# Kernel tuning notes

Hardware: AMD Instinct MI355X
Metric: run time of the kernel (lower is better)

## Reference

```python
import jax, jax.numpy as jnp
import numpy as np

B, N, D = 8, 2048, 256      # batch, tokens, model dim (= out_token_dims)
S = 128                     # query_key_dims
H = int(2.0 * D)            # expansion_factor * D = 512
EPS = 1e-5


def setup_inputs() -> dict:
    key = jax.random.key(0)
    ks = jax.random.split(key, 4)
    x = jax.random.normal(ks[0], (B, N, D), dtype=jnp.float32)
    g = jnp.ones((), jnp.float32)                                # ScaleNorm gain
    W_uv = jax.random.normal(ks[1], (D, 2 * H + S), jnp.float32) * 0.02
    b_uv = jnp.zeros((2 * H + S,), jnp.float32)
    gamma = jnp.ones((2, S), jnp.float32)                        # OffsetScale scale
    beta = jnp.zeros((2, S), jnp.float32)                        # OffsetScale offset
    W_o = jax.random.normal(ks[2], (H, D), jnp.float32) * 0.02
    b_o = jnp.zeros((D,), jnp.float32)
    return {"x": x, "g": g, "W_uv": W_uv, "b_uv": b_uv,
            "gamma": gamma, "beta": beta, "W_o": W_o, "b_o": b_o}


def reference(x, g, W_uv, b_uv, gamma, beta, W_o, b_o):
    d = x.shape[-1]
    # ScaleNorm: x / max(||x|| / sqrt(d), eps) * g
    norm = jnp.linalg.norm(x, axis=-1, keepdims=True) * jax.lax.rsqrt(jnp.float32(d))
    xn = x / jnp.maximum(norm, EPS) * g
    # fused uv projection + SiLU
    uv = jax.nn.silu(jnp.einsum('bnd,de->bne', xn, W_uv) + b_uv)
    u = uv[..., :H]            # gate branch        [B,N,H]
    v = uv[..., H:2 * H]       # value branch       [B,N,H]
    base = uv[..., 2 * H:]     # shared q/k base    [B,N,S]
    # OffsetScale heads=2 -> q, k (cheap per-dim affine)
    q = base * gamma[0] + beta[0]
    k = base * gamma[1] + beta[1]
    # single-head scores + ReLU^2 attention activation
    qk = jnp.einsum('bns,bms->bnm', q, k) * jax.lax.rsqrt(jnp.float32(S))
    attn = jnp.square(jax.nn.relu(qk))
    # gate * (attn @ v), then output projection back to D
    gated = u * jnp.einsum('bnm,bmh->bnh', attn, v)
    return jnp.einsum('bnh,hd->bnd', gated, W_o) + b_o
```

## Files before the change

### kernel.cpp

```cpp
#include <hip/hip_runtime.h>
#include <math.h>

#define BB 8
#define NN 2048
#define DD 256
#define SS 128
#define HH 512
#define EE 1152

typedef short bf16x8 __attribute__((ext_vector_type(8)));
typedef float f32x4 __attribute__((ext_vector_type(4)));

__device__ __forceinline__ short f2bf(float f) {
    union { float f; unsigned u; } a; a.f = f;
    unsigned r = a.u + 0x7FFFu + ((a.u >> 16) & 1u);
    return (short)(r >> 16);
}
__device__ __forceinline__ float bf2f(short s) {
    union { unsigned u; float f; } a; a.u = ((unsigned)(unsigned short)s) << 16;
    return a.f;
}

__global__ __launch_bounds__(256) void k_pre(
        const float* __restrict__ x, const float* __restrict__ gp,
        short* __restrict__ xn,
        const float* __restrict__ Wuv, const float* __restrict__ Wo,
        short* __restrict__ Wuv_t, short* __restrict__ Wo_t) {
    int bid = blockIdx.x;
    if (bid < 4096) {
        int wave = threadIdx.x >> 6, lane = threadIdx.x & 63;
        long row = (long)bid * 4 + wave;
        float4 xv = ((const float4*)(x + row * DD))[lane];
        float ss = xv.x*xv.x + xv.y*xv.y + xv.z*xv.z + xv.w*xv.w;
        #pragma unroll
        for (int off = 32; off > 0; off >>= 1) ss += __shfl_down(ss, off);
        ss = __shfl(ss, 0);
        float norm = sqrtf(ss) * 0.0625f;
        float scale = gp[0] / fmaxf(norm, 1e-5f);
        short4 o;
        o.x = f2bf(xv.x * scale); o.y = f2bf(xv.y * scale);
        o.z = f2bf(xv.z * scale); o.w = f2bf(xv.w * scale);
        ((short4*)(xn + row * DD))[lane] = o;
    } else {
        int idx = (bid - 4096) * 256 + threadIdx.x;
        if (idx < DD * EE) {
            int d = idx / EE, e = idx % EE;
            Wuv_t[e * DD + d] = f2bf(Wuv[idx]);
        }
        int i2 = idx - DD * EE;
        if (i2 >= 0 && i2 < HH * DD) {
            int h = i2 / DD, d = i2 % DD;
            Wo_t[d * HH + h] = f2bf(Wo[i2]);
        }
    }
}

__global__ __launch_bounds__(256) void k_gemm1(
        const short* __restrict__ xn, const short* __restrict__ Wuv_t,
        const float* __restrict__ b_uv,
        const float* __restrict__ gamma, const float* __restrict__ beta,
        short* __restrict__ u, short* __restrict__ v,
        short* __restrict__ q, short* __restrict__ k) {
    __shared__ short As[64][72];
    __shared__ short Bs[64][72];
    int m0 = blockIdx.x * 64, n0 = blockIdx.y * 64;
    int t = threadIdx.x, w = t >> 6, lane = t & 63;
    int wr = w & 1, wc = w >> 1, l16 = lane & 15, quad = lane >> 4;
    int srow = t >> 3, sch = (t & 7) * 8;
    f32x4 acc[2][2] = {};
    for (int k0 = 0; k0 < DD; k0 += 64) {
        __syncthreads();
        *(bf16x8*)&As[srow][sch]    = *(const bf16x8*)&xn[(long)(m0+srow)*DD + k0 + sch];
        *(bf16x8*)&As[srow+32][sch] = *(const bf16x8*)&xn[(long)(m0+srow+32)*DD + k0 + sch];
        *(bf16x8*)&Bs[srow][sch]    = *(const bf16x8*)&Wuv_t[(long)(n0+srow)*DD + k0 + sch];
        *(bf16x8*)&Bs[srow+32][sch] = *(const bf16x8*)&Wuv_t[(long)(n0+srow+32)*DD + k0 + sch];
        __syncthreads();
        #pragma unroll
        for (int kk = 0; kk < 2; kk++) {
            bf16x8 a0 = *(const bf16x8*)&As[wr*32 +      l16][kk*32 + quad*8];
            bf16x8 a1 = *(const bf16x8*)&As[wr*32 + 16 + l16][kk*32 + quad*8];
            bf16x8 b0 = *(const bf16x8*)&Bs[wc*32 +      l16][kk*32 + quad*8];
            bf16x8 b1 = *(const bf16x8*)&Bs[wc*32 + 16 + l16][kk*32 + quad*8];
            acc[0][0] = __builtin_amdgcn_mfma_f32_16x16x32_bf16(a0, b0, acc[0][0], 0,0,0);
            acc[0][1] = __builtin_amdgcn_mfma_f32_16x16x32_bf16(a0, b1, acc[0][1], 0,0,0);
            acc[1][0] = __builtin_amdgcn_mfma_f32_16x16x32_bf16(a1, b0, acc[1][0], 0,0,0);
            acc[1][1] = __builtin_amdgcn_mfma_f32_16x16x32_bf16(a1, b1, acc[1][1], 0,0,0);
        }
    }
    #pragma unroll
    for (int mt = 0; mt < 2; mt++)
    #pragma unroll
    for (int nt = 0; nt < 2; nt++)
    #pragma unroll
    for (int r = 0; r < 4; r++) {
        int gm = m0 + wr*32 + mt*16 + quad*4 + r;
        int ge = n0 + wc*32 + nt*16 + l16;
        float val = acc[mt][nt][r] + b_uv[ge];
        val = val / (1.0f + __expf(-val));
        if (ge < HH) {
            u[(long)gm*HH + ge] = f2bf(val);
        } else if (ge < 2*HH) {
            v[(long)gm*HH + (ge - HH)] = f2bf(val);
        } else {
            int si = ge - 2*HH;
            q[(long)gm*SS + si] = f2bf(val * gamma[si]      + beta[si]);
            k[(long)gm*SS + si] = f2bf(val * gamma[SS + si] + beta[SS + si]);
        }
    }
}

__global__ __launch_bounds__(256) void k_vfrag(
        const short* __restrict__ v, short* __restrict__ vfrag) {
    __shared__ short tile[32][520];
    int mt = blockIdx.x, b = blockIdx.y;
    int t = threadIdx.x;
    const short* vb = v + ((long)b * NN + mt * 32) * HH;
    #pragma unroll
    for (int i = 0; i < 8; i++) {
        int c = t + i * 256, r = c >> 6, co = (c & 63) * 8;
        *(bf16x8*)&tile[r][co] = *(const bf16x8*)&vb[(long)r * HH + co];
    }
    __syncthreads();
    short* dstb = vfrag + (((long)b * 64 + mt) * 32) * 512;
    #pragma unroll
    for (int i = 0; i < 8; i++) {
        int c = t + i * 256, ht = c >> 6, l = c & 63;
        int quad = l >> 4, l16 = l & 15;
        bf16x8 o;
        #pragma unroll
        for (int e = 0; e < 8; e++) o[e] = tile[quad*8 + e][ht*16 + l16];
        *(bf16x8*)&dstb[(long)ht * 512 + l * 8] = o;
    }
}

__global__ __launch_bounds__(512, 2) void k_attn(
        const short* __restrict__ q, const short* __restrict__ k,
        const short* __restrict__ vfrag, const short* __restrict__ u,
        short* __restrict__ gated) {
    __shared__ short ks[2][32][136];
    __shared__ short Ps[2][64][40];
    int b = blockIdx.x & 7;
    int i0 = (blockIdx.x >> 3) * 64;
    int t = threadIdx.x, w = t >> 6, lane = t & 63;
    int l16 = lane & 15, quad = lane >> 4;
    int qt = w >> 1, mt = w & 1;
    const short* qb  = q + ((long)b * NN + i0) * SS;
    const short* kb  = k + (long)b * NN * SS;
    const short* vfb = vfrag + (long)b * 64 * 32 * 512;
    const float RS = 0.08838834764831845f;

    int krow = t >> 4, kch = (t & 15) * 8;

    bf16x8 qf[4];
    #pragma unroll
    for (int kc = 0; kc < 4; kc++)
        qf[kc] = *(const bf16x8*)&qb[(long)(qt*16 + l16)*SS + kc*32 + quad*8];

    *(bf16x8*)&ks[0][krow][kch] = *(const bf16x8*)&kb[(long)krow*SS + kch];
    bf16x8 kpre = *(const bf16x8*)&kb[(long)(32 + krow)*SS + kch];
    __syncthreads();

    f32x4 acc[16] = {};
    for (int it = 0; it < NN/32; it++) {
        int p = it & 1;
        int m0 = it * 32;
        int mnext = (m0 + 64 < NN) ? m0 + 64 : m0;
        bf16x8 knext = *(const bf16x8*)&kb[(long)(mnext + krow)*SS + kch];
        bf16x8 vf[4];
        #pragma unroll
        for (int jj = 0; jj < 4; jj++)
            vf[jj] = *(const bf16x8*)&vfb[((long)it*32 + (w*4 + jj))*512 + lane*8];
        f32x4 sc = {};
        #pragma unroll
        for (int kc = 0; kc < 4; kc++) {
            bf16x8 kf = *(const bf16x8*)&ks[p][mt*16 + l16][kc*32 + quad*8];
            sc = __builtin_amdgcn_mfma_f32_16x16x32_bf16(kf, qf[kc], sc, 0,0,0);
        }
        short4 pw;
        {
            float s0 = fmaxf(sc[0]*RS, 0.f), s1 = fmaxf(sc[1]*RS, 0.f);
            float s2 = fmaxf(sc[2]*RS, 0.f), s3 = fmaxf(sc[3]*RS, 0.f);
            pw.x = f2bf(s0*s0); pw.y = f2bf(s1*s1);
            pw.z = f2bf(s2*s2); pw.w = f2bf(s3*s3);
        }
        *(short4*)&Ps[p][qt*16 + l16][mt*16 + quad*4] = pw;
        *(bf16x8*)&ks[p^1][krow][kch] = kpre;
        kpre = knext;
        __syncthreads();
        bf16x8 af[4];
        #pragma unroll
        for (int qq2 = 0; qq2 < 4; qq2++)
            af[qq2] = *(const bf16x8*)&Ps[p][qq2*16 + l16][quad*8];
        #pragma unroll
        for (int jj = 0; jj < 4; jj++)
            #pragma unroll
            for (int qq2 = 0; qq2 < 4; qq2++)
                acc[qq2*4 + jj] = __builtin_amdgcn_mfma_f32_16x16x32_bf16(
                    af[qq2], vf[jj], acc[qq2*4 + jj], 0,0,0);
    }

    long rowbase = (long)b * NN + i0;
    #pragma unroll
    for (int qq2 = 0; qq2 < 4; qq2++)
    #pragma unroll
    for (int jj = 0; jj < 4; jj++) {
        int gh = (w*4 + jj)*16 + l16;
        #pragma unroll
        for (int r = 0; r < 4; r++) {
            long grow = rowbase + qq2*16 + quad*4 + r;
            float uval = bf2f(u[grow * HH + gh]);
            gated[grow * HH + gh] = f2bf(acc[qq2*4 + jj][r] * uval);
        }
    }
}

__global__ __launch_bounds__(256) void k_gemm2(
        const short* __restrict__ gated, const short* __restrict__ Wo_t,
        const float* __restrict__ b_o, float* __restrict__ out) {
    __shared__ short As[64][72];
    __shared__ short Bs[64][72];
    int m0 = blockIdx.x * 64, n0 = blockIdx.y * 64;
    int t = threadIdx.x, w = t >> 6, lane = t & 63;
    int wr = w & 1, wc = w >> 1, l16 = lane & 15, quad = lane >> 4;
    int srow = t >> 3, sch = (t & 7) * 8;
    f32x4 acc[2][2] = {};
    for (int k0 = 0; k0 < HH; k0 += 64) {
        __syncthreads();
        *(bf16x8*)&As[srow][sch]    = *(const bf16x8*)&gated[(long)(m0+srow)*HH + k0 + sch];
        *(bf16x8*)&As[srow+32][sch] = *(const bf16x8*)&gated[(long)(m0+srow+32)*HH + k0 + sch];
        *(bf16x8*)&Bs[srow][sch]    = *(const bf16x8*)&Wo_t[(long)(n0+srow)*HH + k0 + sch];
        *(bf16x8*)&Bs[srow+32][sch] = *(const bf16x8*)&Wo_t[(long)(n0+srow+32)*HH + k0 + sch];
        __syncthreads();
        #pragma unroll
        for (int kk = 0; kk < 2; kk++) {
            bf16x8 a0 = *(const bf16x8*)&As[wr*32 +      l16][kk*32 + quad*8];
            bf16x8 a1 = *(const bf16x8*)&As[wr*32 + 16 + l16][kk*32 + quad*8];
            bf16x8 b0 = *(const bf16x8*)&Bs[wc*32 +      l16][kk*32 + quad*8];
            bf16x8 b1 = *(const bf16x8*)&Bs[wc*32 + 16 + l16][kk*32 + quad*8];
            acc[0][0] = __builtin_amdgcn_mfma_f32_16x16x32_bf16(a0, b0, acc[0][0], 0,0,0);
            acc[0][1] = __builtin_amdgcn_mfma_f32_16x16x32_bf16(a0, b1, acc[0][1], 0,0,0);
            acc[1][0] = __builtin_amdgcn_mfma_f32_16x16x32_bf16(a1, b0, acc[1][0], 0,0,0);
            acc[1][1] = __builtin_amdgcn_mfma_f32_16x16x32_bf16(a1, b1, acc[1][1], 0,0,0);
        }
    }
    #pragma unroll
    for (int mt = 0; mt < 2; mt++)
    #pragma unroll
    for (int nt = 0; nt < 2; nt++)
    #pragma unroll
    for (int r = 0; r < 4; r++) {
        int gm = m0 + wr*32 + mt*16 + quad*4 + r;
        int gd = n0 + wc*32 + nt*16 + l16;
        out[(long)gm*DD + gd] = acc[mt][nt][r] + b_o[gd];
    }
}

extern "C" void kernel_launch(void* const* d_in, const int* in_sizes, int n_in,
                              void* d_out, int out_size, void* d_ws, size_t ws_size,
                              hipStream_t stream) {
    const float* x     = (const float*)d_in[0];
    const float* g     = (const float*)d_in[1];
    const float* Wuv   = (const float*)d_in[2];
    const float* b_uv  = (const float*)d_in[3];
    const float* gamma = (const float*)d_in[4];
    const float* beta  = (const float*)d_in[5];
    const float* Wo    = (const float*)d_in[6];
    const float* b_o   = (const float*)d_in[7];
    float* out = (float*)d_out;

    short* ws    = (short*)d_ws;
    short* xn    = ws;
    short* Wuv_t = xn    + (long)16384 * 256;
    short* Wo_t  = Wuv_t + (long)1152 * 256;
    short* u     = Wo_t  + (long)256 * 512;
    short* v     = u     + (long)16384 * 512;
    short* vfrag = v     + (long)16384 * 512;
    short* qq    = vfrag + (long)16384 * 512;
    short* kk    = qq    + (long)16384 * 128;
    short* gated = kk    + (long)16384 * 128;

    k_pre<<<5760, 256, 0, stream>>>(x, g, xn, Wuv, Wo, Wuv_t, Wo_t);
    k_gemm1<<<dim3(256, 18), 256, 0, stream>>>(xn, Wuv_t, b_uv, gamma, beta, u, v, qq, kk);
    k_vfrag<<<dim3(64, 8), 256, 0, stream>>>(v, vfrag);
    k_attn<<<256, 512, 0, stream>>>(qq, kk, vfrag, u, gated);
    k_gemm2<<<dim3(256, 4), 256, 0, stream>>>(gated, Wo_t, b_o, out);
}
```

Measured before the change: 174.1 us.

## Tile weight transposes, enlarge GEMM tiles with direct-to-LDS loads, double-step attention loop

The weight-transpose path now goes through a 32x32 shared-memory tile, so both reads and writes are coalesced. Both projection GEMMs move from 64x64 to 128x128 tiles, load operands with global_load_lds straight into unpadded LDS, and issue 16 MFMAs per wave per k-step. The attention loop handles two 32-key chunks per iteration and prefetches V fragments one step ahead, which halves the number of barriers. The unpadded LDS layout may cause bank conflicts, and the larger tiles launch fewer blocks (1152 for gemm1, 256 for gemm2), which can lower occupancy.

Measured after the change: 182.3 us. +4.7%, slower.

```diff
diff --git a/kernel.cpp b/kernel.cpp
--- a/kernel.cpp
+++ b/kernel.cpp
@@ -20,15 +20,22 @@
     union { unsigned u; float f; } a; a.u = ((unsigned)(unsigned short)s) << 16;
     return a.f;
 }
+__device__ __forceinline__ void gl_lds16(const short* g, short* l) {
+    __builtin_amdgcn_global_load_lds(
+        (const __attribute__((address_space(1))) void*)g,
+        (__attribute__((address_space(3))) void*)l, 16, 0, 0);
+}
 
 __global__ __launch_bounds__(256) void k_pre(
         const float* __restrict__ x, const float* __restrict__ gp,
         short* __restrict__ xn,
         const float* __restrict__ Wuv, const float* __restrict__ Wo,
         short* __restrict__ Wuv_t, short* __restrict__ Wo_t) {
+    __shared__ float tile[32][33];
     int bid = blockIdx.x;
+    int t = threadIdx.x;
     if (bid < 4096) {
-        int wave = threadIdx.x >> 6, lane = threadIdx.x & 63;
+        int wave = t >> 6, lane = t & 63;
         long row = (long)bid * 4 + wave;
         float4 xv = ((const float4*)(x + row * DD))[lane];
         float ss = xv.x*xv.x + xv.y*xv.y + xv.z*xv.z + xv.w*xv.w;
@@ -41,16 +48,33 @@
         o.x = f2bf(xv.x * scale); o.y = f2bf(xv.y * scale);
         o.z = f2bf(xv.z * scale); o.w = f2bf(xv.w * scale);
         ((short4*)(xn + row * DD))[lane] = o;
+    } else if (bid < 4384) {
+        int bid2 = bid - 4096;
+        int et = bid2 % 36, dt = bid2 / 36;
+        #pragma unroll
+        for (int i = 0; i < 4; i++) {
+            int idx = t + i*256, r = idx >> 5, c = idx & 31;
+            tile[r][c] = Wuv[(long)(dt*32 + r)*EE + et*32 + c];
+        }
+        __syncthreads();
+        #pragma unroll
+        for (int i = 0; i < 4; i++) {
+            int idx = t + i*256, r = idx >> 5, c = idx & 31;
+            Wuv_t[(long)(et*32 + r)*DD + dt*32 + c] = f2bf(tile[c][r]);
+        }
     } else {
-        int idx = (bid - 4096) * 256 + threadIdx.x;
-        if (idx < DD * EE) {
-            int d = idx / EE, e = idx % EE;
-            Wuv_t[e * DD + d] = f2bf(Wuv[idx]);
-        }
-        int i2 = idx - DD * EE;
-        if (i2 >= 0 && i2 < HH * DD) {
-            int h = i2 / DD, d = i2 % DD;
-            Wo_t[d * HH + h] = f2bf(Wo[i2]);
+        int bid3 = bid - 4384;
+        int ht = bid3 % 16, dt = bid3 / 16;
+        #pragma unroll
+        for (int i = 0; i < 4; i++) {
+            int idx = t + i*256, r = idx >> 5, c = idx & 31;
+            tile[r][c] = Wo[(long)(ht*32 + r)*DD + dt*32 + c];
+        }
+        __syncthreads();
+        #pragma unroll
+        for (int i = 0; i < 4; i++) {
+            int idx = t + i*256, r = idx >> 5, c = idx & 31;
+            Wo_t[(long)(dt*32 + r)*HH + ht*32 + c] = f2bf(tile[c][r]);
         }
     }
 }
@@ -61,40 +85,47 @@
         const float* __restrict__ gamma, const float* __restrict__ beta,
         short* __restrict__ u, short* __restrict__ v,
         short* __restrict__ q, short* __restrict__ k) {
-    __shared__ short As[64][72];
-    __shared__ short Bs[64][72];
-    int m0 = blockIdx.x * 64, n0 = blockIdx.y * 64;
+    __shared__ short As[128*64];
+    __shared__ short Bs[128*64];
+    int m0 = blockIdx.x * 128, n0 = blockIdx.y * 128;
     int t = threadIdx.x, w = t >> 6, lane = t & 63;
     int wr = w & 1, wc = w >> 1, l16 = lane & 15, quad = lane >> 4;
-    int srow = t >> 3, sch = (t & 7) * 8;
-    f32x4 acc[2][2] = {};
+    int lr = lane >> 3, lc = (lane & 7) * 8;
+    f32x4 acc[4][4] = {};
     for (int k0 = 0; k0 < DD; k0 += 64) {
         __syncthreads();
-        *(bf16x8*)&As[srow][sch]    = *(const bf16x8*)&xn[(long)(m0+srow)*DD + k0 + sch];
-        *(bf16x8*)&As[srow+32][sch] = *(const bf16x8*)&xn[(long)(m0+srow+32)*DD + k0 + sch];
-        *(bf16x8*)&Bs[srow][sch]    = *(const bf16x8*)&Wuv_t[(long)(n0+srow)*DD + k0 + sch];
-        *(bf16x8*)&Bs[srow+32][sch] = *(const bf16x8*)&Wuv_t[(long)(n0+srow+32)*DD + k0 + sch];
+        #pragma unroll
+        for (int i = 0; i < 4; i++) {
+            int r0 = i*32 + w*8;
+            gl_lds16(&xn[(long)(m0 + r0 + lr)*DD + k0 + lc], &As[r0*64]);
+            gl_lds16(&Wuv_t[(long)(n0 + r0 + lr)*DD + k0 + lc], &Bs[r0*64]);
+        }
         __syncthreads();
         #pragma unroll
         for (int kk = 0; kk < 2; kk++) {
-            bf16x8 a0 = *(const bf16x8*)&As[wr*32 +      l16][kk*32 + quad*8];
-            bf16x8 a1 = *(const bf16x8*)&As[wr*32 + 16 + l16][kk*32 + quad*8];
-            bf16x8 b0 = *(const bf16x8*)&Bs[wc*32 +      l16][kk*32 + quad*8];
-            bf16x8 b1 = *(const bf16x8*)&Bs[wc*32 + 16 + l16][kk*32 + quad*8];
-            acc[0][0] = __builtin_amdgcn_mfma_f32_16x16x32_bf16(a0, b0, acc[0][0], 0,0,0);
-            acc[0][1] = __builtin_amdgcn_mfma_f32_16x16x32_bf16(a0, b1, acc[0][1], 0,0,0);
-            acc[1][0] = __builtin_amdgcn_mfma_f32_16x16x32_bf16(a1, b0, acc[1][0], 0,0,0);
-            acc[1][1] = __builtin_amdgcn_mfma_f32_16x16x32_bf16(a1, b1, acc[1][1], 0,0,0);
-        }
-    }
-    #pragma unroll
-    for (int mt = 0; mt < 2; mt++)
-    #pragma unroll
-    for (int nt = 0; nt < 2; nt++)
+            bf16x8 a[4], bb[4];
+            #pragma unroll
+            for (int mt = 0; mt < 4; mt++)
+                a[mt] = *(const bf16x8*)&As[(wr*64 + mt*16 + l16)*64 + kk*32 + quad*8];
+            #pragma unroll
+            for (int nt = 0; nt < 4; nt++)
+                bb[nt] = *(const bf16x8*)&Bs[(wc*64 + nt*16 + l16)*64 + kk*32 + quad*8];
+            #pragma unroll
+            for (int mt = 0; mt < 4; mt++)
+                #pragma unroll
+                for (int nt = 0; nt < 4; nt++)
+                    acc[mt][nt] = __builtin_amdgcn_mfma_f32_16x16x32_bf16(
+                        a[mt], bb[nt], acc[mt][nt], 0,0,0);
+        }
+    }
+    #pragma unroll
+    for (int mt = 0; mt < 4; mt++)
+    #pragma unroll
+    for (int nt = 0; nt < 4; nt++)
     #pragma unroll
     for (int r = 0; r < 4; r++) {
-        int gm = m0 + wr*32 + mt*16 + quad*4 + r;
-        int ge = n0 + wc*32 + nt*16 + l16;
+        int gm = m0 + wr*64 + mt*16 + quad*4 + r;
+        int ge = n0 + wc*64 + nt*16 + l16;
         float val = acc[mt][nt][r] + b_uv[ge];
         val = val / (1.0f + __expf(-val));
         if (ge < HH) {
@@ -137,8 +168,8 @@
         const short* __restrict__ q, const short* __restrict__ k,
         const short* __restrict__ vfrag, const short* __restrict__ u,
         short* __restrict__ gated) {
-    __shared__ short ks[2][32][136];
-    __shared__ short Ps[2][64][40];
+    __shared__ short ks[2][2][32][136];
+    __shared__ short Ps[2][2][64][40];
     int b = blockIdx.x & 7;
     int i0 = (blockIdx.x >> 3) * 64;
     int t = threadIdx.x, w = t >> 6, lane = t & 63;
@@ -156,47 +187,77 @@
     for (int kc = 0; kc < 4; kc++)
         qf[kc] = *(const bf16x8*)&qb[(long)(qt*16 + l16)*SS + kc*32 + quad*8];
 
-    *(bf16x8*)&ks[0][krow][kch] = *(const bf16x8*)&kb[(long)krow*SS + kch];
-    bf16x8 kpre = *(const bf16x8*)&kb[(long)(32 + krow)*SS + kch];
+    *(bf16x8*)&ks[0][0][krow][kch] = *(const bf16x8*)&kb[(long)krow*SS + kch];
+    *(bf16x8*)&ks[0][1][krow][kch] = *(const bf16x8*)&kb[(long)(32 + krow)*SS + kch];
+    bf16x8 kpre0 = *(const bf16x8*)&kb[(long)(64 + krow)*SS + kch];
+    bf16x8 kpre1 = *(const bf16x8*)&kb[(long)(96 + krow)*SS + kch];
+    bf16x8 vfc[8];
+    #pragma unroll
+    for (int jj = 0; jj < 4; jj++) {
+        vfc[jj]     = *(const bf16x8*)&vfb[((long)(w*4 + jj))*512 + lane*8];
+        vfc[4 + jj] = *(const bf16x8*)&vfb[((long)(32 + w*4 + jj))*512 + lane*8];
+    }
     __syncthreads();
 
     f32x4 acc[16] = {};
-    for (int it = 0; it < NN/32; it++) {
-        int p = it & 1;
-        int m0 = it * 32;
-        int mnext = (m0 + 64 < NN) ? m0 + 64 : m0;
-        bf16x8 knext = *(const bf16x8*)&kb[(long)(mnext + krow)*SS + kch];
-        bf16x8 vf[4];
-        #pragma unroll
-        for (int jj = 0; jj < 4; jj++)
-            vf[jj] = *(const bf16x8*)&vfb[((long)it*32 + (w*4 + jj))*512 + lane*8];
-        f32x4 sc = {};
+    for (int s = 0; s < 32; s++) {
+        int p = s & 1;
+        int sk = (s + 2 < 32) ? s + 2 : s;
+        bf16x8 kfar0 = *(const bf16x8*)&kb[(long)(sk*64 + krow)*SS + kch];
+        bf16x8 kfar1 = *(const bf16x8*)&kb[(long)(sk*64 + 32 + krow)*SS + kch];
+        int sv = (s + 1 < 32) ? s + 1 : s;
+        bf16x8 vfn[8];
+        #pragma unroll
+        for (int jj = 0; jj < 4; jj++) {
+            vfn[jj]     = *(const bf16x8*)&vfb[((long)(2*sv)*32     + w*4 + jj)*512 + lane*8];
+            vfn[4 + jj] = *(const bf16x8*)&vfb[((long)(2*sv + 1)*32 + w*4 + jj)*512 + lane*8];
+        }
+        f32x4 scA = {}, scB = {};
         #pragma unroll
         for (int kc = 0; kc < 4; kc++) {
-            bf16x8 kf = *(const bf16x8*)&ks[p][mt*16 + l16][kc*32 + quad*8];
-            sc = __builtin_amdgcn_mfma_f32_16x16x32_bf16(kf, qf[kc], sc, 0,0,0);
-        }
-        short4 pw;
+            bf16x8 kfA = *(const bf16x8*)&ks[p][0][mt*16 + l16][kc*32 + quad*8];
+            scA = __builtin_amdgcn_mfma_f32_16x16x32_bf16(kfA, qf[kc], scA, 0,0,0);
+        }
+        #pragma unroll
+        for (int kc = 0; kc < 4; kc++) {
+            bf16x8 kfB = *(const bf16x8*)&ks[p][1][mt*16 + l16][kc*32 + quad*8];
+            scB = __builtin_amdgcn_mfma_f32_16x16x32_bf16(kfB, qf[kc], scB, 0,0,0);
+        }
+        short4 pwA, pwB;
         {
-            float s0 = fmaxf(sc[0]*RS, 0.f), s1 = fmaxf(sc[1]*RS, 0.f);
-            float s2 = fmaxf(sc[2]*RS, 0.f), s3 = fmaxf(sc[3]*RS, 0.f);
-            pw.x = f2bf(s0*s0); pw.y = f2bf(s1*s1);
-            pw.z = f2bf(s2*s2); pw.w = f2bf(s3*s3);
-        }
-        *(short4*)&Ps[p][qt*16 + l16][mt*16 + quad*4] = pw;
-        *(bf16x8*)&ks[p^1][krow][kch] = kpre;
-        kpre = knext;
-        __syncthreads();
-        bf16x8 af[4];
-        #pragma unroll
-        for (int qq2 = 0; qq2 < 4; qq2++)
-            af[qq2] = *(const bf16x8*)&Ps[p][qq2*16 + l16][quad*8];
-        #pragma unroll
-        for (int jj = 0; jj < 4; jj++)
-            #pragma unroll
-            for (int qq2 = 0; qq2 < 4; qq2++)
+            float a0 = fmaxf(scA[0]*RS, 0.f), a1 = fmaxf(scA[1]*RS, 0.f);
+            float a2 = fmaxf(scA[2]*RS, 0.f), a3 = fmaxf(scA[3]*RS, 0.f);
+            pwA.x = f2bf(a0*a0); pwA.y = f2bf(a1*a1);
+            pwA.z = f2bf(a2*a2); pwA.w = f2bf(a3*a3);
+            float b0 = fmaxf(scB[0]*RS, 0.f), b1 = fmaxf(scB[1]*RS, 0.f);
+            float b2 = fmaxf(scB[2]*RS, 0.f), b3 = fmaxf(scB[3]*RS, 0.f);
+            pwB.x = f2bf(b0*b0); pwB.y = f2bf(b1*b1);
+            pwB.z = f2bf(b2*b2); pwB.w = f2bf(b3*b3);
+        }
+        *(short4*)&Ps[p][0][qt*16 + l16][mt*16 + quad*4] = pwA;
+        *(short4*)&Ps[p][1][qt*16 + l16][mt*16 + quad*4] = pwB;
+        *(bf16x8*)&ks[p^1][0][krow][kch] = kpre0;
+        *(bf16x8*)&ks[p^1][1][krow][kch] = kpre1;
+        kpre0 = kfar0; kpre1 = kfar1;
+        __syncthreads();
+        #pragma unroll
+        for (int qq2 = 0; qq2 < 4; qq2++) {
+            bf16x8 afA = *(const bf16x8*)&Ps[p][0][qq2*16 + l16][quad*8];
+            #pragma unroll
+            for (int jj = 0; jj < 4; jj++)
                 acc[qq2*4 + jj] = __builtin_amdgcn_mfma_f32_16x16x32_bf16(
-                    af[qq2], vf[jj], acc[qq2*4 + jj], 0,0,0);
+                    afA, vfc[jj], acc[qq2*4 + jj], 0,0,0);
+        }
+        #pragma unroll
+        for (int qq2 = 0; qq2 < 4; qq2++) {
+            bf16x8 afB = *(const bf16x8*)&Ps[p][1][qq2*16 + l16][quad*8];
+            #pragma unroll
+            for (int jj = 0; jj < 4; jj++)
+                acc[qq2*4 + jj] = __builtin_amdgcn_mfma_f32_16x16x32_bf16(
+                    afB, vfc[4 + jj], acc[qq2*4 + jj], 0,0,0);
+        }
+        #pragma unroll
+        for (int i = 0; i < 8; i++) vfc[i] = vfn[i];
     }
 
     long rowbase = (long)b * NN + i0;
@@ -217,40 +278,47 @@
 __global__ __launch_bounds__(256) void k_gemm2(
         const short* __restrict__ gated, const short* __restrict__ Wo_t,
         const float* __restrict__ b_o, float* __restrict__ out) {
-    __shared__ short As[64][72];
-    __shared__ short Bs[64][72];
-    int m0 = blockIdx.x * 64, n0 = blockIdx.y * 64;
+    __shared__ short As[128*64];
+    __shared__ short Bs[128*64];
+    int m0 = blockIdx.x * 128, n0 = blockIdx.y * 128;
     int t = threadIdx.x, w = t >> 6, lane = t & 63;
     int wr = w & 1, wc = w >> 1, l16 = lane & 15, quad = lane >> 4;
-    int srow = t >> 3, sch = (t & 7) * 8;
-    f32x4 acc[2][2] = {};
+    int lr = lane >> 3, lc = (lane & 7) * 8;
+    f32x4 acc[4][4] = {};
     for (int k0 = 0; k0 < HH; k0 += 64) {
         __syncthreads();
-        *(bf16x8*)&As[srow][sch]    = *(const bf16x8*)&gated[(long)(m0+srow)*HH + k0 + sch];
-        *(bf16x8*)&As[srow+32][sch] = *(const bf16x8*)&gated[(long)(m0+srow+32)*HH + k0 + sch];
-        *(bf16x8*)&Bs[srow][sch]    = *(const bf16x8*)&Wo_t[(long)(n0+srow)*HH + k0 + sch];
-        *(bf16x8*)&Bs[srow+32][sch] = *(const bf16x8*)&Wo_t[(long)(n0+srow+32)*HH + k0 + sch];
+        #pragma unroll
+        for (int i = 0; i < 4; i++) {
+            int r0 = i*32 + w*8;
+            gl_lds16(&gated[(long)(m0 + r0 + lr)*HH + k0 + lc], &As[r0*64]);
+            gl_lds16(&Wo_t[(long)(n0 + r0 + lr)*HH + k0 + lc], &Bs[r0*64]);
+        }
         __syncthreads();
         #pragma unroll
         for (int kk = 0; kk < 2; kk++) {
-            bf16x8 a0 = *(const bf16x8*)&As[wr*32 +      l16][kk*32 + quad*8];
-            bf16x8 a1 = *(const bf16x8*)&As[wr*32 + 16 + l16][kk*32 + quad*8];
-            bf16x8 b0 = *(const bf16x8*)&Bs[wc*32 +      l16][kk*32 + quad*8];
-            bf16x8 b1 = *(const bf16x8*)&Bs[wc*32 + 16 + l16][kk*32 + quad*8];
-            acc[0][0] = __builtin_amdgcn_mfma_f32_16x16x32_bf16(a0, b0, acc[0][0], 0,0,0);
-            acc[0][1] = __builtin_amdgcn_mfma_f32_16x16x32_bf16(a0, b1, acc[0][1], 0,0,0);
-            acc[1][0] = __builtin_amdgcn_mfma_f32_16x16x32_bf16(a1, b0, acc[1][0], 0,0,0);
-            acc[1][1] = __builtin_amdgcn_mfma_f32_16x16x32_bf16(a1, b1, acc[1][1], 0,0,0);
-        }
-    }
-    #pragma unroll
-    for (int mt = 0; mt < 2; mt++)
-    #pragma unroll
-    for (int nt = 0; nt < 2; nt++)
+            bf16x8 a[4], bb[4];
+            #pragma unroll
+            for (int mt = 0; mt < 4; mt++)
+                a[mt] = *(const bf16x8*)&As[(wr*64 + mt*16 + l16)*64 + kk*32 + quad*8];
+            #pragma unroll
+            for (int nt = 0; nt < 4; nt++)
+                bb[nt] = *(const bf16x8*)&Bs[(wc*64 + nt*16 + l16)*64 + kk*32 + quad*8];
+            #pragma unroll
+            for (int mt = 0; mt < 4; mt++)
+                #pragma unroll
+                for (int nt = 0; nt < 4; nt++)
+                    acc[mt][nt] = __builtin_amdgcn_mfma_f32_16x16x32_bf16(
+                        a[mt], bb[nt], acc[mt][nt], 0,0,0);
+        }
+    }
+    #pragma unroll
+    for (int mt = 0; mt < 4; mt++)
+    #pragma unroll
+    for (int nt = 0; nt < 4; nt++)
     #pragma unroll
     for (int r = 0; r < 4; r++) {
-        int gm = m0 + wr*32 + mt*16 + quad*4 + r;
-        int gd = n0 + wc*32 + nt*16 + l16;
+        int gm = m0 + wr*64 + mt*16 + quad*4 + r;
+        int gd = n0 + wc*64 + nt*16 + l16;
         out[(long)gm*DD + gd] = acc[mt][nt][r] + b_o[gd];
     }
 }
@@ -279,9 +347,9 @@
     short* kk    = qq    + (long)16384 * 128;
     short* gated = kk    + (long)16384 * 128;
 
-    k_pre<<<5760, 256, 0, stream>>>(x, g, xn, Wuv, Wo, Wuv_t, Wo_t);
-    k_gemm1<<<dim3(256, 18), 256, 0, stream>>>(xn, Wuv_t, b_uv, gamma, beta, u, v, qq, kk);
+    k_pre<<<4512, 256, 0, stream>>>(x, g, xn, Wuv, Wo, Wuv_t, Wo_t);
+    k_gemm1<<<dim3(128, 9), 256, 0, stream>>>(xn, Wuv_t, b_uv, gamma, beta, u, v, qq, kk);
     k_vfrag<<<dim3(64, 8), 256, 0, stream>>>(v, vfrag);
     k_attn<<<256, 512, 0, stream>>>(qq, kk, vfrag, u, gated);
-    k_gemm2<<<dim3(256, 4), 256, 0, stream>>>(gated, Wo_t, b_o, out);
-}
+    k_gemm2<<<dim3(128, 2), 256, 0, stream>>>(gated, Wo_t, b_o, out);
+}
```
